# Performance work log

Measured on AMD Instinct MI355X. Metric: run time of the kernel, lower is better.

Reference implementation:

```python
import jax, jax.numpy as jnp
import numpy as np

B, S, D = 32, 1024, 256
K, H, L = 64, 4, 4
KH, DV = K // H, D // H  # pooling key size per head, pooling value size
EPS = 1e-5
SCALE = 1.0 / np.sqrt(K).astype(np.float32)  # both encoder and pooling use sqrt(1/key_size)


def _ln(x, gamma=None, beta=None):
    m = jnp.mean(x, axis=-1, keepdims=True)
    v = jnp.mean(jnp.square(x - m), axis=-1, keepdims=True)
    y = (x - m) * jax.lax.rsqrt(v + EPS)
    if gamma is not None:
        y = y * gamma + beta
    return y


def setup_inputs() -> dict:
    key = jax.random.key(0)
    ks = iter(jax.random.split(key, 32))

    def w(shape, fan_in):
        return jax.random.normal(next(ks), shape, jnp.float32) / np.sqrt(fan_in).astype(np.float32)

    inp = {
        "input": jax.random.normal(next(ks), (B, S, D), jnp.float32),
        "lin0_W": w((D, D), D), "lin0_b": jnp.zeros((D,), jnp.float32),
        # stacked params for the 4 AttentionEncoder layers
        "enc_Wk": w((L, D, K), D), "enc_bk": jnp.zeros((L, K), jnp.float32),
        "enc_Wq": w((L, D, K), D), "enc_bq": jnp.zeros((L, K), jnp.float32),
        "enc_Wv": w((L, D, D), D), "enc_bv": jnp.zeros((L, D), jnp.float32),
        "enc_Wb": w((L, D, 1), D), "enc_bb": jnp.zeros((L, 1), jnp.float32),
        "enc_Wff": w((L, D, D), D), "enc_bff": jnp.zeros((L, D), jnp.float32),
        "enc_g1": jnp.ones((L, D), jnp.float32), "enc_beta1": jnp.zeros((L, D), jnp.float32),
        # multi-head pooling head
        "pool_Wk": w((D, KH), D), "pool_bk": jnp.zeros((KH,), jnp.float32),
        "pool_Wv": w((D, DV), D), "pool_bv": jnp.zeros((DV,), jnp.float32),
        "queries": jax.random.normal(next(ks), (H, KH), jnp.float32),
        "lin1_W": w((D, 2), D), "lin1_b": jnp.zeros((2,), jnp.float32),
    }
    return inp


def reference(input, lin0_W, lin0_b, enc_Wk, enc_bk, enc_Wq, enc_bq, enc_Wv, enc_bv,
              enc_Wb, enc_bb, enc_Wff, enc_bff, enc_g1, enc_beta1,
              pool_Wk, pool_bk, pool_Wv, pool_bv, queries, lin1_W, lin1_b):
    # NOTE: original code computes act0(lin0(input)) and then discards it (dead code);
    # it is omitted here since it does not affect the output.
    x = input
    for i in range(L):
        k = (x @ enc_Wk[i] + enc_bk[i]) * SCALE          # [B,S,K]
        q = x @ enc_Wq[i] + enc_bq[i]                     # [B,S,K]
        v = x @ enc_Wv[i] + enc_bv[i]                     # [B,S,D]
        bias = x @ enc_Wb[i] + enc_bb[i]                  # [B,S,1], broadcast over columns
        scores = jax.nn.sigmoid(jnp.einsum('bik,bjk->bij', k, q) + bias)  # [B,S,S]
        attn = jnp.einsum('bij,bjd->bid', scores, v)      # [B,S,D]
        res = _ln(x + attn, enc_g1[i], enc_beta1[i])
        ff = jax.nn.relu(res @ enc_Wff[i] + enc_bff[i])
        x = _ln(res + ff)                                 # norm2: no affine
    # multi-head pooling with learned queries
    pk = (x @ pool_Wk + pool_bk) * SCALE                  # [B,S,KH]
    pv = x @ pool_Wv + pool_bv                            # [B,S,DV]
    sc = jnp.einsum('bsk,hk->bsh', pk, queries)           # [B,S,H]
    sc = jax.nn.softmax(sc, axis=1)                       # softmax over sequence
    pooled = jnp.einsum('bsh,bsd->bhd', sc, pv).reshape(x.shape[0], -1)  # [B, H*DV]=[B,D]
    return pooled @ lin1_W + lin1_b                       # [B,2]
```

## Files before the change

kernel.cpp:

```cpp
#include <hip/hip_runtime.h>
#include <hip/hip_bf16.h>
#include <math.h>

#define BB 32
#define SS 1024
#define DD 256
#define MM (BB*SS)
#define LEPS 1e-5f

typedef __bf16 bf16x8 __attribute__((ext_vector_type(8)));
typedef __bf16 bf16x4 __attribute__((ext_vector_type(4)));
typedef float f32x4 __attribute__((ext_vector_type(4)));

__global__ __launch_bounds__(256) void cast_wt(const float* __restrict__ W,
                                               __bf16* __restrict__ WT,
                                               int N, float scale, int dstride, int noff) {
    int n = blockIdx.x, l = blockIdx.z, k = threadIdx.x;
    WT[(size_t)dstride * l + (size_t)(n + noff) * 256 + k] =
        (__bf16)(W[(size_t)256 * N * l + (size_t)k * N + n] * scale);
}

__global__ __launch_bounds__(128) void bias_combine(const float* __restrict__ bk,
                                                    const float* __restrict__ bq,
                                                    float* __restrict__ dst) {
    int l = blockIdx.x, j = threadIdx.x;
    dst[l * 128 + j] = (j < 64) ? bk[l * 64 + j] * 0.125f : bq[l * 64 + (j - 64)];
}

__global__ __launch_bounds__(256) void cast_x(const float* __restrict__ x, __bf16* __restrict__ xb) {
    size_t i = ((size_t)blockIdx.x * 256 + threadIdx.x) * 8;
    float4 a = *(const float4*)(x + i);
    float4 b = *(const float4*)(x + i + 4);
    __bf16 o[8] __attribute__((aligned(16)));
    o[0] = (__bf16)a.x; o[1] = (__bf16)a.y; o[2] = (__bf16)a.z; o[3] = (__bf16)a.w;
    o[4] = (__bf16)b.x; o[5] = (__bf16)b.y; o[6] = (__bf16)b.z; o[7] = (__bf16)b.w;
    *(bf16x8*)(xb + i) = *(bf16x8*)o;
}

template <int BN, int MODE>
__global__ __launch_bounds__(256) void gemm_mfma(const __bf16* __restrict__ A,
                                                 const __bf16* __restrict__ WT,
                                                 const float* __restrict__ bias,
                                                 float bscale, int relu,
                                                 void* __restrict__ Cv, void* __restrict__ Cv2,
                                                 int N) {
    constexpr int MR = (BN == 128) ? 4 : 2;
    constexpr int NC = (BN == 128) ? 4 : BN / 16;
    const int t = threadIdx.x;
    const int w = t >> 6, lane = t & 63;
    const int m0 = blockIdx.x * 128;
    const int n0 = blockIdx.y * BN;
    const size_t wt_z = (MODE == 3) ? (size_t)blockIdx.z * SS * 256 : 0;
    const size_t c_z  = (MODE == 3) ? (size_t)blockIdx.z * 256 * (size_t)N : 0;
    const int wr = (BN == 128) ? (w >> 1) * 64 : w * 32;
    const int wc = (BN == 128) ? (w & 1) * 64 : 0;
    __shared__ __align__(16) __bf16 Al[128][64];
    __shared__ __align__(16) __bf16 Wl[BN][64];
    f32x4 acc[MR][NC] = {};

    for (int k0 = 0; k0 < 256; k0 += 64) {
        __syncthreads();
        {
            int r = t >> 1, half = t & 1;
            const __bf16* src = A + (size_t)(m0 + r) * 256 + k0 + half * 32;
            bf16x8 v0 = *(const bf16x8*)(src);
            bf16x8 v1 = *(const bf16x8*)(src + 8);
            bf16x8 v2 = *(const bf16x8*)(src + 16);
            bf16x8 v3 = *(const bf16x8*)(src + 24);
            int cb = half * 4;
            *(bf16x8*)&Al[r][((cb + 0) ^ (r & 7)) * 8] = v0;
            *(bf16x8*)&Al[r][((cb + 1) ^ (r & 7)) * 8] = v1;
            *(bf16x8*)&Al[r][((cb + 2) ^ (r & 7)) * 8] = v2;
            *(bf16x8*)&Al[r][((cb + 3) ^ (r & 7)) * 8] = v3;
        }
        if (BN == 128) {
            int r = t >> 1, half = t & 1;
            const __bf16* src = WT + wt_z + (size_t)(n0 + r) * 256 + k0 + half * 32;
            bf16x8 v0 = *(const bf16x8*)(src);
            bf16x8 v1 = *(const bf16x8*)(src + 8);
            bf16x8 v2 = *(const bf16x8*)(src + 16);
            bf16x8 v3 = *(const bf16x8*)(src + 24);
            int cb = half * 4;
            *(bf16x8*)&Wl[r][((cb + 0) ^ (r & 7)) * 8] = v0;
            *(bf16x8*)&Wl[r][((cb + 1) ^ (r & 7)) * 8] = v1;
            *(bf16x8*)&Wl[r][((cb + 2) ^ (r & 7)) * 8] = v2;
            *(bf16x8*)&Wl[r][((cb + 3) ^ (r & 7)) * 8] = v3;
        } else if (BN == 64) {
            int n = t >> 2, q = t & 3;
            const __bf16* src = WT + (size_t)(n0 + n) * 256 + k0 + q * 16;
            bf16x8 v0 = *(const bf16x8*)src;
            bf16x8 v1 = *(const bf16x8*)(src + 8);
            *(bf16x8*)&Wl[n][((q * 2 + 0) ^ (n & 7)) * 8] = v0;
            *(bf16x8*)&Wl[n][((q * 2 + 1) ^ (n & 7)) * 8] = v1;
        } else {
            if (t < 128) {
                int n = t >> 3, c = t & 7;
                bf16x8 v = *(const bf16x8*)(WT + (size_t)(n0 + n) * 256 + k0 + c * 8);
                *(bf16x8*)&Wl[n][(c ^ (n & 7)) * 8] = v;
            }
        }
        __syncthreads();
#pragma unroll
        for (int ks = 0; ks < 2; ks++) {
            int c = ks * 4 + (lane >> 4);
            bf16x8 af[MR];
#pragma unroll
            for (int mf = 0; mf < MR; mf++) {
                int i = wr + mf * 16 + (lane & 15);
                af[mf] = *(const bf16x8*)&Al[i][(c ^ (i & 7)) * 8];
            }
#pragma unroll
            for (int nf = 0; nf < NC; nf++) {
                int n = wc + nf * 16 + (lane & 15);
                bf16x8 bfr = *(const bf16x8*)&Wl[n][(c ^ (n & 7)) * 8];
#pragma unroll
                for (int mf = 0; mf < MR; mf++)
                    acc[mf][nf] = __builtin_amdgcn_mfma_f32_16x16x32_bf16(af[mf], bfr, acc[mf][nf], 0, 0, 0);
            }
        }
    }
#pragma unroll
    for (int mf = 0; mf < MR; mf++) {
#pragma unroll
        for (int nf = 0; nf < NC; nf++) {
            int col = n0 + wc + nf * 16 + (lane & 15);
            float bcol = (MODE == 3) ? 0.f : bias[col] * bscale;
#pragma unroll
            for (int r = 0; r < 4; r++) {
                int row = m0 + wr + mf * 16 + (lane >> 4) * 4 + r;
                float v = acc[mf][nf][r] + ((MODE == 3) ? bias[row] : bcol);
                if (relu) v = fmaxf(v, 0.f);
                if (MODE == 2) {
                    if (col < 64) ((__bf16*)Cv)[(size_t)row * 64 + col] = (__bf16)v;
                    else ((__bf16*)Cv2)[(size_t)row * 64 + (col - 64)] = (__bf16)v;
                } else if (MODE == 1 || MODE == 3) {
                    ((__bf16*)Cv)[c_z + (size_t)row * N + col] = (__bf16)v;
                } else {
                    ((float*)Cv)[(size_t)row * N + col] = v;
                }
            }
        }
    }
}

__global__ __launch_bounds__(256) void bias_gemv(const __bf16* __restrict__ X,
                                                 const float* __restrict__ Wb,
                                                 const float* __restrict__ bb,
                                                 float* __restrict__ out) {
    int wave = threadIdx.x >> 6, lane = threadIdx.x & 63;
    size_t row = (size_t)blockIdx.x * 4 + wave;
    bf16x4 xv = *(const bf16x4*)(X + row * 256 + lane * 4);
    float4 wv = *(const float4*)(Wb + lane * 4);
    float p = (float)xv[0] * wv.x + (float)xv[1] * wv.y + (float)xv[2] * wv.z + (float)xv[3] * wv.w;
    for (int off = 32; off; off >>= 1) p += __shfl_down(p, off, 64);
    if (lane == 0) out[row] = p + bb[0];
}

__global__ __launch_bounds__(512, 4) void attn_mfma(const __bf16* __restrict__ kb,
                                                    const __bf16* __restrict__ qb,
                                                    const __bf16* __restrict__ vT,
                                                    const float* __restrict__ biasb,
                                                    const float* __restrict__ xin,
                                                    const float* __restrict__ gamma,
                                                    const float* __restrict__ beta,
                                                    float* __restrict__ outf,
                                                    __bf16* __restrict__ outb) {
    int h = blockIdx.x;
    int blow = h & 7, rest = h >> 3;
    int ib = rest & 15;
    int b = blow + (rest >> 4) * 8;
    const int i0 = ib * 64;
    const int t = threadIdx.x;
    const int w = t >> 6, lane = t & 63;
    const int iq = w >> 1;
    const int dhalf = w & 1;

    __shared__ __align__(16) __bf16 Kl[64][64];
    __shared__ __align__(16) __bf16 Ql[64][64];
    __shared__ __align__(16) __bf16 Vl[256][64];
    __shared__ __align__(16) __bf16 Sl[64][64];
    __shared__ float bsh[64];
    __shared__ float rowred[2][64][2];

    const int qj = t >> 3, qc = t & 7;
    const __bf16* qsrc_base = qb + ((size_t)(b * SS + qj)) * 64 + qc * 8;
    const int vd = t >> 1, vjh = t & 1;
    const __bf16* vsrc_base = vT + ((size_t)b * 256 + vd) * SS + vjh * 32;

    {
        int i = t >> 3, c = t & 7;
        bf16x8 v = *(const bf16x8*)(kb + ((size_t)(b * SS + i0 + i)) * 64 + c * 8);
        *(bf16x8*)&Kl[i][(c ^ (i & 7)) * 8] = v;
        if (t < 64) bsh[t] = biasb[b * SS + i0 + t];
    }
    {
        bf16x8 qv = *(const bf16x8*)(qsrc_base);
        *(bf16x8*)&Ql[qj][(qc ^ (qj & 7)) * 8] = qv;
#pragma unroll
        for (int u = 0; u < 4; u++) {
            bf16x8 v = *(const bf16x8*)(vsrc_base + u * 8);
            *(bf16x8*)&Vl[vd][((vjh * 4 + u) ^ (vd & 7)) * 8] = v;
        }
    }
    __syncthreads();

    f32x4 acc[8] = {};

    for (int j0 = 0; j0 < SS; j0 += 64) {
        const bool has_next = (j0 + 64) < SS;
        bf16x8 qn;
        bf16x8 vn0, vn1, vn2, vn3;
        if (has_next) {
            qn = *(const bf16x8*)(qsrc_base + (size_t)(j0 + 64) * 64);
            const __bf16* vs = vsrc_base + j0 + 64;
            vn0 = *(const bf16x8*)(vs);
            vn1 = *(const bf16x8*)(vs + 8);
            vn2 = *(const bf16x8*)(vs + 16);
            vn3 = *(const bf16x8*)(vs + 24);
        }
#pragma unroll
        for (int jj = 0; jj < 2; jj++) {
            int jq = (w & 1) * 2 + jj;
            f32x4 sacc = {0.f, 0.f, 0.f, 0.f};
            __builtin_amdgcn_s_setprio(1);
#pragma unroll
            for (int ks = 0; ks < 2; ks++) {
                int i = iq * 16 + (lane & 15);
                int ck = ks * 4 + (lane >> 4);
                bf16x8 a = *(const bf16x8*)&Kl[i][(ck ^ (i & 7)) * 8];
                int j = jq * 16 + (lane & 15);
                bf16x8 bq = *(const bf16x8*)&Ql[j][(ck ^ (j & 7)) * 8];
                sacc = __builtin_amdgcn_mfma_f32_16x16x32_bf16(a, bq, sacc, 0, 0, 0);
            }
            __builtin_amdgcn_s_setprio(0);
            int jcol = jq * 16 + (lane & 15);
#pragma unroll
            for (int r = 0; r < 4; r++) {
                int irow = iq * 16 + (lane >> 4) * 4 + r;
                float x = sacc[r] + bsh[irow];
                float sg = 1.f / (1.f + __expf(-x));
                Sl[irow][(((jcol >> 3) ^ (irow & 7)) * 8) + (jcol & 7)] = (__bf16)sg;
            }
        }
        __syncthreads();
        bf16x8 am[2];
#pragma unroll
        for (int m = 0; m < 2; m++) {
            int i = iq * 16 + (lane & 15);
            int cj = m * 4 + (lane >> 4);
            am[m] = *(const bf16x8*)&Sl[i][(cj ^ (i & 7)) * 8];
        }
        __builtin_amdgcn_s_setprio(1);
#pragma unroll
        for (int dq = 0; dq < 8; dq++) {
            int d = dhalf * 128 + dq * 16 + (lane & 15);
#pragma unroll
            for (int m = 0; m < 2; m++) {
                int cj = m * 4 + (lane >> 4);
                bf16x8 bv = *(const bf16x8*)&Vl[d][(cj ^ (d & 7)) * 8];
                acc[dq] = __builtin_amdgcn_mfma_f32_16x16x32_bf16(am[m], bv, acc[dq], 0, 0, 0);
            }
        }
        __builtin_amdgcn_s_setprio(0);
        __syncthreads();
        if (has_next) {
            *(bf16x8*)&Ql[qj][(qc ^ (qj & 7)) * 8] = qn;
            *(bf16x8*)&Vl[vd][((vjh * 4 + 0) ^ (vd & 7)) * 8] = vn0;
            *(bf16x8*)&Vl[vd][((vjh * 4 + 1) ^ (vd & 7)) * 8] = vn1;
            *(bf16x8*)&Vl[vd][((vjh * 4 + 2) ^ (vd & 7)) * 8] = vn2;
            *(bf16x8*)&Vl[vd][((vjh * 4 + 3) ^ (vd & 7)) * 8] = vn3;
            __syncthreads();
        }
    }

#pragma unroll
    for (int r = 0; r < 4; r++) {
        int il = iq * 16 + (lane >> 4) * 4 + r;
        size_t rowoff = ((size_t)(b * SS + i0 + il)) * 256 + dhalf * 128 + (lane & 15);
#pragma unroll
        for (int dq = 0; dq < 8; dq++)
            acc[dq][r] += xin[rowoff + dq * 16];
    }
    float sr[4], qr[4];
#pragma unroll
    for (int r = 0; r < 4; r++) {
        float s = 0.f, q = 0.f;
#pragma unroll
        for (int dq = 0; dq < 8; dq++) {
            float v = acc[dq][r];
            s += v; q += v * v;
        }
#pragma unroll
        for (int mask = 8; mask; mask >>= 1) {
            s += __shfl_xor(s, mask, 64);
            q += __shfl_xor(q, mask, 64);
        }
        sr[r] = s; qr[r] = q;
    }
    if ((lane & 15) == 0) {
#pragma unroll
        for (int r = 0; r < 4; r++) {
            int il = iq * 16 + (lane >> 4) * 4 + r;
            rowred[dhalf][il][0] = sr[r];
            rowred[dhalf][il][1] = qr[r];
        }
    }
    __syncthreads();
    float gv[8], bv2[8];
#pragma unroll
    for (int dq = 0; dq < 8; dq++) {
        int d = dhalf * 128 + dq * 16 + (lane & 15);
        gv[dq] = gamma[d];
        bv2[dq] = beta[d];
    }
#pragma unroll
    for (int r = 0; r < 4; r++) {
        int il = iq * 16 + (lane >> 4) * 4 + r;
        float st = rowred[0][il][0] + rowred[1][il][0];
        float qt = rowred[0][il][1] + rowred[1][il][1];
        float mean = st * (1.f / 256.f);
        float var = qt * (1.f / 256.f) - mean * mean;
        float inv = 1.f / sqrtf(var + LEPS);
        size_t rowoff = ((size_t)(b * SS + i0 + il)) * 256 + dhalf * 128 + (lane & 15);
#pragma unroll
        for (int dq = 0; dq < 8; dq++) {
            float o = (acc[dq][r] - mean) * inv * gv[dq] + bv2[dq];
            outf[rowoff + dq * 16] = o;
            outb[rowoff + dq * 16] = (__bf16)o;
        }
    }
}

__global__ __launch_bounds__(512) void gemm_ff_ln2(const __bf16* __restrict__ A,
                                                   const __bf16* __restrict__ WT,
                                                   const float* __restrict__ bias,
                                                   const float* __restrict__ resid,
                                                   float* __restrict__ outf,
                                                   __bf16* __restrict__ outb) {
    const int t = threadIdx.x;
    const int w = t >> 6, lane = t & 63;
    const int m0 = blockIdx.x * 128;
    const int wr = (w >> 2) * 64, wc = (w & 3) * 64;
    __shared__ __align__(16) __bf16 Al[128][64];
    __shared__ __align__(16) __bf16 Wl[256][64];
    __shared__ float rowred[4][128][2];
    f32x4 acc[4][4] = {};

    for (int k0 = 0; k0 < 256; k0 += 64) {
        __syncthreads();
        {
            int r = t >> 2, c0 = (t & 3) * 2;
            const __bf16* src = A + (size_t)(m0 + r) * 256 + k0 + c0 * 8;
            bf16x8 v0 = *(const bf16x8*)src;
            bf16x8 v1 = *(const bf16x8*)(src + 8);
            *(bf16x8*)&Al[r][((c0 + 0) ^ (r & 7)) * 8] = v0;
            *(bf16x8*)&Al[r][((c0 + 1) ^ (r & 7)) * 8] = v1;
        }
        {
            int n = t >> 1, c0 = (t & 1) * 4;
            const __bf16* src = WT + (size_t)n * 256 + k0 + c0 * 8;
#pragma unroll
            for (int u = 0; u < 4; u++) {
                bf16x8 v = *(const bf16x8*)(src + u * 8);
                *(bf16x8*)&Wl[n][((c0 + u) ^ (n & 7)) * 8] = v;
            }
        }
        __syncthreads();
#pragma unroll
        for (int ks = 0; ks < 2; ks++) {
            int c = ks * 4 + (lane >> 4);
            bf16x8 af[4];
#pragma unroll
            for (int mf = 0; mf < 4; mf++) {
                int i = wr + mf * 16 + (lane & 15);
                af[mf] = *(const bf16x8*)&Al[i][(c ^ (i & 7)) * 8];
            }
#pragma unroll
            for (int nf = 0; nf < 4; nf++) {
                int n = wc + nf * 16 + (lane & 15);
                bf16x8 bfr = *(const bf16x8*)&Wl[n][(c ^ (n & 7)) * 8];
#pragma unroll
                for (int mf = 0; mf < 4; mf++)
                    acc[mf][nf] = __builtin_amdgcn_mfma_f32_16x16x32_bf16(af[mf], bfr, acc[mf][nf], 0, 0, 0);
            }
        }
    }
    float colb[4];
#pragma unroll
    for (int nf = 0; nf < 4; nf++) colb[nf] = bias[wc + nf * 16 + (lane & 15)];
#pragma unroll
    for (int mf = 0; mf < 4; mf++) {
#pragma unroll
        for (int r = 0; r < 4; r++) {
            int rl = wr + mf * 16 + (lane >> 4) * 4 + r;
            const float* rrow = resid + (size_t)(m0 + rl) * 256 + wc + (lane & 15);
            float s = 0.f, q = 0.f;
#pragma unroll
            for (int nf = 0; nf < 4; nf++) {
                float v = fmaxf(acc[mf][nf][r] + colb[nf], 0.f) + rrow[nf * 16];
                acc[mf][nf][r] = v;
                s += v; q += v * v;
            }
#pragma unroll
            for (int msk = 1; msk <= 8; msk <<= 1) {
                s += __shfl_xor(s, msk, 64);
                q += __shfl_xor(q, msk, 64);
            }
            if ((lane & 15) == 0) {
                rowred[w & 3][rl][0] = s;
                rowred[w & 3][rl][1] = q;
            }
        }
    }
    __syncthreads();
#pragma unroll
    for (int mf = 0; mf < 4; mf++) {
#pragma unroll
        for (int r = 0; r < 4; r++) {
            int rl = wr + mf * 16 + (lane >> 4) * 4 + r;
            float s = rowred[0][rl][0] + rowred[1][rl][0] + rowred[2][rl][0] + rowred[3][rl][0];
            float q = rowred[0][rl][1] + rowred[1][rl][1] + rowred[2][rl][1] + rowred[3][rl][1];
            float mean = s * (1.f / 256.f);
            float var = q * (1.f / 256.f) - mean * mean;
            float inv = 1.f / sqrtf(var + LEPS);
            size_t base = (size_t)(m0 + rl) * 256 + wc + (lane & 15);
#pragma unroll
            for (int nf = 0; nf < 4; nf++) {
                float o = (acc[mf][nf][r] - mean) * inv;
                outf[base + nf * 16] = o;
                outb[base + nf * 16] = (__bf16)o;
            }
        }
    }
}

__global__ __launch_bounds__(256) void pool_kernel(const float* __restrict__ pk,
                                                   const float* __restrict__ pv,
                                                   const float* __restrict__ queries,
                                                   const float* __restrict__ W1,
                                                   const float* __restrict__ b1,
                                                   float* __restrict__ out) {
    const int b = blockIdx.x;
    const int t = threadIdx.x;
    __shared__ float sc[4][1024];
    __shared__ float qv[4][16];
    __shared__ float redsum[4];
    __shared__ float r0[256], r1[256];
    if (t < 64) qv[t >> 4][t & 15] = queries[t];
    __syncthreads();
    for (int c = 0; c < 4; c++) {
        int s = c * 256 + t;
        const float* p = pk + ((size_t)b * SS + s) * 16;
        float4 a0 = *(const float4*)p;
        float4 a1 = *(const float4*)(p + 4);
        float4 a2 = *(const float4*)(p + 8);
        float4 a3 = *(const float4*)(p + 12);
#pragma unroll
        for (int hh = 0; hh < 4; hh++) {
            float d = a0.x * qv[hh][0] + a0.y * qv[hh][1] + a0.z * qv[hh][2] + a0.w * qv[hh][3]
                    + a1.x * qv[hh][4] + a1.y * qv[hh][5] + a1.z * qv[hh][6] + a1.w * qv[hh][7]
                    + a2.x * qv[hh][8] + a2.y * qv[hh][9] + a2.z * qv[hh][10] + a2.w * qv[hh][11]
                    + a3.x * qv[hh][12] + a3.y * qv[hh][13] + a3.z * qv[hh][14] + a3.w * qv[hh][15];
            sc[hh][s] = d;
        }
    }
    __syncthreads();
    {
        int hh = t >> 6, lane = t & 63;
        float m = -1e30f;
        for (int s = lane; s < 1024; s += 64) m = fmaxf(m, sc[hh][s]);
        for (int off = 32; off; off >>= 1) m = fmaxf(m, __shfl_down(m, off, 64));
        m = __shfl(m, 0, 64);
        float sum = 0.f;
        for (int s = lane; s < 1024; s += 64) {
            float e = expf(sc[hh][s] - m);
            sc[hh][s] = e;
            sum += e;
        }
        for (int off = 32; off; off >>= 1) sum += __shfl_down(sum, off, 64);
        if (lane == 0) redsum[hh] = sum;
    }
    __syncthreads();
    int hh = t >> 6, d = t & 63;
    float acc = 0.f;
    for (int s = 0; s < 1024; s++) acc += sc[hh][s] * pv[((size_t)b * SS + s) * 64 + d];
    acc /= redsum[hh];
    float p0 = acc * W1[t * 2 + 0];
    float p1 = acc * W1[t * 2 + 1];
    r0[t] = p0; r1[t] = p1;
    __syncthreads();
    for (int off = 128; off > 0; off >>= 1) {
        if (t < off) { r0[t] += r0[t + off]; r1[t] += r1[t + off]; }
        __syncthreads();
    }
    if (t == 0) {
        out[b * 2 + 0] = r0[0] + b1[0];
        out[b * 2 + 1] = r1[0] + b1[1];
    }
}

extern "C" void kernel_launch(void* const* d_in, const int* in_sizes, int n_in,
                              void* d_out, int out_size, void* d_ws, size_t ws_size,
                              hipStream_t stream) {
    const float* input = (const float*)d_in[0];
    const float* eWk = (const float*)d_in[3];
    const float* ebk = (const float*)d_in[4];
    const float* eWq = (const float*)d_in[5];
    const float* ebq = (const float*)d_in[6];
    const float* eWv = (const float*)d_in[7];
    const float* ebv = (const float*)d_in[8];
    const float* eWb = (const float*)d_in[9];
    const float* ebb = (const float*)d_in[10];
    const float* eWff = (const float*)d_in[11];
    const float* ebff = (const float*)d_in[12];
    const float* eg1 = (const float*)d_in[13];
    const float* ebe1 = (const float*)d_in[14];
    const float* pWk = (const float*)d_in[15];
    const float* pbk = (const float*)d_in[16];
    const float* pWv = (const float*)d_in[17];
    const float* pbv = (const float*)d_in[18];
    const float* qrs = (const float*)d_in[19];
    const float* W1 = (const float*)d_in[20];
    const float* b1 = (const float*)d_in[21];
    float* out = (float*)d_out;

    float* ws = (float*)d_ws;
    float* xbuf = ws;
    __bf16* xbf = (__bf16*)(xbuf + (size_t)MM * DD);
    float* tmp2 = (float*)(xbf + (size_t)MM * DD);
    float* r3 = tmp2 + (size_t)MM * DD;
    __bf16* tmp2bf = (__bf16*)r3;
    __bf16* vTb = tmp2bf + (size_t)MM * DD;
    float* r4 = r3 + (size_t)MM * DD;
    __bf16* kbf = (__bf16*)r4;
    __bf16* qbf = kbf + (size_t)MM * 64;
    float* bbuf = r4 + (size_t)MM * (DD / 2);
    __bf16* wbf = (__bf16*)(bbuf + MM);

    __bf16* WkqT = wbf;
    __bf16* WvT = WkqT + 4 * 128 * 256;
    __bf16* WffT = WvT + 4 * 256 * 256;
    __bf16* pWkT = WffT + 4 * 256 * 256;
    __bf16* pWvT = pWkT + 16 * 256;
    float* biasc = (float*)(pWvT + 64 * 256);

    float* pkbuf = tmp2;
    float* pvbuf = tmp2 + (size_t)MM * 16;

    const float SC = 0.125f;

    cast_wt<<<dim3(64, 1, 4), 256, 0, stream>>>(eWk, WkqT, 64, SC, 128 * 256, 0);
    cast_wt<<<dim3(64, 1, 4), 256, 0, stream>>>(eWq, WkqT, 64, 1.f, 128 * 256, 64);
    cast_wt<<<dim3(256, 1, 4), 256, 0, stream>>>(eWv, WvT, 256, 1.f, 256 * 256, 0);
    cast_wt<<<dim3(256, 1, 4), 256, 0, stream>>>(eWff, WffT, 256, 1.f, 256 * 256, 0);
    cast_wt<<<dim3(16, 1, 1), 256, 0, stream>>>(pWk, pWkT, 16, SC, 16 * 256, 0);
    cast_wt<<<dim3(64, 1, 1), 256, 0, stream>>>(pWv, pWvT, 64, 1.f, 64 * 256, 0);
    bias_combine<<<4, 128, 0, stream>>>(ebk, ebq, biasc);
    cast_x<<<MM * DD / (256 * 8), 256, 0, stream>>>(input, xbf);

    for (int l = 0; l < 4; l++) {
        const float* xin = (l == 0) ? input : xbuf;
        gemm_mfma<128, 2><<<dim3(MM / 128, 1), 256, 0, stream>>>(
            xbf, WkqT + (size_t)l * 128 * 256, biasc + l * 128, 1.f, 0, kbf, qbf, 64);
        gemm_mfma<128, 3><<<dim3(2, SS / 128, BB), 256, 0, stream>>>(
            WvT + (size_t)l * 256 * 256, xbf, ebv + l * DD, 1.f, 0, vTb, nullptr, SS);
        bias_gemv<<<MM / 4, 256, 0, stream>>>(xbf, eWb + (size_t)l * DD, ebb + l, bbuf);
        attn_mfma<<<dim3(512, 1), 512, 0, stream>>>(kbf, qbf, vTb, bbuf, xin,
                                                    eg1 + l * DD, ebe1 + l * DD, tmp2, tmp2bf);
        gemm_ff_ln2<<<dim3(MM / 128, 1), 512, 0, stream>>>(
            tmp2bf, WffT + (size_t)l * 256 * 256, ebff + l * DD, tmp2, xbuf, xbf);
    }
    gemm_mfma<16, 0><<<dim3(MM / 128, 1), 256, 0, stream>>>(xbf, pWkT, pbk, SC, 0, pkbuf, nullptr, 16);
    gemm_mfma<64, 0><<<dim3(MM / 128, 1), 256, 0, stream>>>(xbf, pWvT, pbv, 1.f, 0, pvbuf, nullptr, 64);
    pool_kernel<<<BB, 256, 0, stream>>>(pkbuf, pvbuf, qrs, W1, b1, out);
}
```

Before: 485.7 us.

## Carry residual stream in bf16 only and widen pooling kernel to 1024 threads

The fp32 residual copies that attention and the FF+LN kernels wrote are dropped. Both residual adds now read the bf16 activation buffers, which cuts global write and read traffic per layer. The pooling kernel runs with 1024 threads, splitting the sequence reduction into four chunks that are summed in shared memory. The cost is lower accuracy, since the residual path is rounded to bf16 at every layer.

After: 488.0 us. Within noise of the previous version (+0.5%).

```diff
diff --git a/kernel.cpp b/kernel.cpp
--- a/kernel.cpp
+++ b/kernel.cpp
@@ -160,10 +160,9 @@
                                                     const __bf16* __restrict__ qb,
                                                     const __bf16* __restrict__ vT,
                                                     const float* __restrict__ biasb,
-                                                    const float* __restrict__ xin,
+                                                    const __bf16* __restrict__ xinb,
                                                     const float* __restrict__ gamma,
                                                     const float* __restrict__ beta,
-                                                    float* __restrict__ outf,
                                                     __bf16* __restrict__ outb) {
     int h = blockIdx.x;
     int blow = h & 7, rest = h >> 3;
@@ -279,7 +278,7 @@
         size_t rowoff = ((size_t)(b * SS + i0 + il)) * 256 + dhalf * 128 + (lane & 15);
 #pragma unroll
         for (int dq = 0; dq < 8; dq++)
-            acc[dq][r] += xin[rowoff + dq * 16];
+            acc[dq][r] += (float)xinb[rowoff + dq * 16];
     }
     float sr[4], qr[4];
 #pragma unroll
@@ -325,7 +324,6 @@
 #pragma unroll
         for (int dq = 0; dq < 8; dq++) {
             float o = (acc[dq][r] - mean) * inv * gv[dq] + bv2[dq];
-            outf[rowoff + dq * 16] = o;
             outb[rowoff + dq * 16] = (__bf16)o;
         }
     }
@@ -334,8 +332,7 @@
 __global__ __launch_bounds__(512) void gemm_ff_ln2(const __bf16* __restrict__ A,
                                                    const __bf16* __restrict__ WT,
                                                    const float* __restrict__ bias,
-                                                   const float* __restrict__ resid,
-                                                   float* __restrict__ outf,
+                                                   const __bf16* __restrict__ resid,
                                                    __bf16* __restrict__ outb) {
     const int t = threadIdx.x;
     const int w = t >> 6, lane = t & 63;
@@ -393,11 +390,11 @@
 #pragma unroll
         for (int r = 0; r < 4; r++) {
             int rl = wr + mf * 16 + (lane >> 4) * 4 + r;
-            const float* rrow = resid + (size_t)(m0 + rl) * 256 + wc + (lane & 15);
+            const __bf16* rrow = resid + (size_t)(m0 + rl) * 256 + wc + (lane & 15);
             float s = 0.f, q = 0.f;
 #pragma unroll
             for (int nf = 0; nf < 4; nf++) {
-                float v = fmaxf(acc[mf][nf][r] + colb[nf], 0.f) + rrow[nf * 16];
+                float v = fmaxf(acc[mf][nf][r] + colb[nf], 0.f) + (float)rrow[nf * 16];
                 acc[mf][nf][r] = v;
                 s += v; q += v * v;
             }
@@ -427,29 +424,29 @@
 #pragma unroll
             for (int nf = 0; nf < 4; nf++) {
                 float o = (acc[mf][nf][r] - mean) * inv;
-                outf[base + nf * 16] = o;
                 outb[base + nf * 16] = (__bf16)o;
             }
         }
     }
 }
 
-__global__ __launch_bounds__(256) void pool_kernel(const float* __restrict__ pk,
-                                                   const float* __restrict__ pv,
-                                                   const float* __restrict__ queries,
-                                                   const float* __restrict__ W1,
-                                                   const float* __restrict__ b1,
-                                                   float* __restrict__ out) {
+__global__ __launch_bounds__(1024) void pool_kernel(const float* __restrict__ pk,
+                                                    const float* __restrict__ pv,
+                                                    const float* __restrict__ queries,
+                                                    const float* __restrict__ W1,
+                                                    const float* __restrict__ b1,
+                                                    float* __restrict__ out) {
     const int b = blockIdx.x;
     const int t = threadIdx.x;
     __shared__ float sc[4][1024];
     __shared__ float qv[4][16];
     __shared__ float redsum[4];
+    __shared__ float psum[4][256];
     __shared__ float r0[256], r1[256];
     if (t < 64) qv[t >> 4][t & 15] = queries[t];
     __syncthreads();
-    for (int c = 0; c < 4; c++) {
-        int s = c * 256 + t;
+    {
+        int s = t;
         const float* p = pk + ((size_t)b * SS + s) * 16;
         float4 a0 = *(const float4*)p;
         float4 a1 = *(const float4*)(p + 4);
@@ -465,7 +462,7 @@
         }
     }
     __syncthreads();
-    {
+    if (t < 256) {
         int hh = t >> 6, lane = t & 63;
         float m = -1e30f;
         for (int s = lane; s < 1024; s += 64) m = fmaxf(m, sc[hh][s]);
@@ -481,13 +478,21 @@
         if (lane == 0) redsum[hh] = sum;
     }
     __syncthreads();
-    int hh = t >> 6, d = t & 63;
-    float acc = 0.f;
-    for (int s = 0; s < 1024; s++) acc += sc[hh][s] * pv[((size_t)b * SS + s) * 64 + d];
-    acc /= redsum[hh];
-    float p0 = acc * W1[t * 2 + 0];
-    float p1 = acc * W1[t * 2 + 1];
-    r0[t] = p0; r1[t] = p1;
+    {
+        int chunk = t >> 8, pair = t & 255;
+        int hh = pair >> 6, d = pair & 63;
+        float a = 0.f;
+        int s0 = chunk * 256;
+        for (int s = s0; s < s0 + 256; s++)
+            a += sc[hh][s] * pv[((size_t)b * SS + s) * 64 + d];
+        psum[chunk][pair] = a;
+    }
+    __syncthreads();
+    if (t < 256) {
+        float a = (psum[0][t] + psum[1][t] + psum[2][t] + psum[3][t]) / redsum[t >> 6];
+        r0[t] = a * W1[t * 2 + 0];
+        r1[t] = a * W1[t * 2 + 1];
+    }
     __syncthreads();
     for (int off = 128; off > 0; off >>= 1) {
         if (t < off) { r0[t] += r0[t + off]; r1[t] += r1[t + off]; }
@@ -559,18 +564,17 @@
     cast_x<<<MM * DD / (256 * 8), 256, 0, stream>>>(input, xbf);
 
     for (int l = 0; l < 4; l++) {
-        const float* xin = (l == 0) ? input : xbuf;
         gemm_mfma<128, 2><<<dim3(MM / 128, 1), 256, 0, stream>>>(
             xbf, WkqT + (size_t)l * 128 * 256, biasc + l * 128, 1.f, 0, kbf, qbf, 64);
         gemm_mfma<128, 3><<<dim3(2, SS / 128, BB), 256, 0, stream>>>(
             WvT + (size_t)l * 256 * 256, xbf, ebv + l * DD, 1.f, 0, vTb, nullptr, SS);
         bias_gemv<<<MM / 4, 256, 0, stream>>>(xbf, eWb + (size_t)l * DD, ebb + l, bbuf);
-        attn_mfma<<<dim3(512, 1), 512, 0, stream>>>(kbf, qbf, vTb, bbuf, xin,
-                                                    eg1 + l * DD, ebe1 + l * DD, tmp2, tmp2bf);
+        attn_mfma<<<dim3(512, 1), 512, 0, stream>>>(kbf, qbf, vTb, bbuf, xbf,
+                                                    eg1 + l * DD, ebe1 + l * DD, tmp2bf);
         gemm_ff_ln2<<<dim3(MM / 128, 1), 512, 0, stream>>>(
-            tmp2bf, WffT + (size_t)l * 256 * 256, ebff + l * DD, tmp2, xbuf, xbf);
+            tmp2bf, WffT + (size_t)l * 256 * 256, ebff + l * DD, tmp2bf, xbf);
     }
     gemm_mfma<16, 0><<<dim3(MM / 128, 1), 256, 0, stream>>>(xbf, pWkT, pbk, SC, 0, pkbuf, nullptr, 16);
     gemm_mfma<64, 0><<<dim3(MM / 128, 1), 256, 0, stream>>>(xbf, pWvT, pbv, 1.f, 0, pvbuf, nullptr, 64);
-    pool_kernel<<<BB, 256, 0, stream>>>(pkbuf, pvbuf, qrs, W1, b1, out);
-}
+    pool_kernel<<<BB, 1024, 0, stream>>>(pkbuf, pvbuf, qrs, W1, b1, out);
+}
```
